# Kernel tuning notes

Measured on AMD Instinct MI355X. Metric: run time of the kernel, lower is better.

## Reference

```python
import jax, jax.numpy as jnp
import numpy as np

C = 256
B = 8
N = 2048
EPS_BN = 1e-5


def _bn(x, g, b):
    # BatchNorm1d in training mode: stats over (batch, length) per channel
    m = x.mean(axis=(0, 2), keepdims=True)
    v = ((x - m) ** 2).mean(axis=(0, 2), keepdims=True)
    return g[None, :, None] * (x - m) / jnp.sqrt(v + EPS_BN) + b[None, :, None]


def _sa_layer(x, wqk, wv, bv, wt, bt, g, b):
    # shared q/k projection (q_conv.weight = k_conv.weight in the original)
    q = jnp.einsum('oc,bcn->bon', wqk, x)          # [B, C//4, N]
    energy = jnp.einsum('bcm,bcn->bmn', q, q)      # x_q^T x_k -> [B, N, N]
    att = jax.nn.softmax(energy, axis=-1)
    att = att / (1e-9 + att.sum(axis=1, keepdims=True))  # L1 renorm over dim=1
    v = jnp.einsum('oc,bcn->bon', wv, x) + bv[None, :, None]
    x_r = jnp.einsum('bcm,bmn->bcn', v, att)       # [B, C, N]
    t = jnp.einsum('oc,bcn->bon', wt, x - x_r) + bt[None, :, None]
    x_r = jax.nn.relu(_bn(t, g, b))
    return x + x_r


def setup_inputs() -> dict:
    key = jax.random.key(0)
    ks = jax.random.split(key, 16)
    s = lambda k, shp, scale: jax.random.normal(k, shp, dtype=jnp.float32) * scale
    inp = {
        'x': s(ks[0], (B, C, N), 1.0),
        'conv1_w': s(ks[1], (C, C), 1.0 / np.sqrt(C)),
        'conv2_w': s(ks[2], (C, C), 1.0 / np.sqrt(C)),
        'bn1_g': jnp.ones((C,), jnp.float32),
        'bn1_b': jnp.zeros((C,), jnp.float32),
        'bn2_g': jnp.ones((C,), jnp.float32),
        'bn2_b': jnp.zeros((C,), jnp.float32),
        'sa_wqk': s(ks[3], (4, C // 4, C), 1.0 / np.sqrt(C)),
        'sa_wv': s(ks[4], (4, C, C), 1.0 / np.sqrt(C)),
        'sa_bv': s(ks[5], (4, C), 0.01),
        'sa_wt': s(ks[6], (4, C, C), 1.0 / np.sqrt(C)),
        'sa_bt': s(ks[7], (4, C), 0.01),
        'sa_g': jnp.ones((4, C), jnp.float32),
        'sa_b': jnp.zeros((4, C), jnp.float32),
    }
    return inp


def reference(x, conv1_w, conv2_w, bn1_g, bn1_b, bn2_g, bn2_b,
              sa_wqk, sa_wv, sa_bv, sa_wt, sa_bt, sa_g, sa_b):
    x = jax.nn.relu(_bn(jnp.einsum('oc,bcn->bon', conv1_w, x), bn1_g, bn1_b))
    x = jax.nn.relu(_bn(jnp.einsum('oc,bcn->bon', conv2_w, x), bn2_g, bn2_b))
    outs = []
    for i in range(4):  # four structurally identical SA layers, small fixed loop
        x = _sa_layer(x, sa_wqk[i], sa_wv[i], sa_bv[i], sa_wt[i], sa_bt[i],
                      sa_g[i], sa_b[i])
        outs.append(x)
    return jnp.concatenate(outs, axis=1)  # [B, 4*C, N]
```

## Files before the change

### kernel.cpp

```cpp
#include <hip/hip_runtime.h>
#include <hip/hip_bf16.h>

typedef __attribute__((ext_vector_type(8))) short short8;
typedef __attribute__((ext_vector_type(4))) float f32x4;
using bf16 = __hip_bfloat16;

constexpr int C  = 256;
constexpr int BB = 8;
constexpr int NN = 2048;

#define DEVI __device__ __forceinline__

DEVI short8 ldg8(const bf16* p) { return *reinterpret_cast<const short8*>(p); }

DEVI f32x4 mfma16(short8 a, short8 b, f32x4 c) {
  return __builtin_amdgcn_mfma_f32_16x16x32_bf16(a, b, c, 0, 0, 0);
}

DEVI void split2(float x, bf16& h, bf16& l) {
  h = __float2bfloat16(x);
  l = __float2bfloat16(x - __bfloat162float(h));
}

DEVI short b2s(bf16 x) { short s; __builtin_memcpy(&s, &x, 2); return s; }


DEVI void store_tile16(const float v[4], bf16* __restrict__ H, bf16* __restrict__ L,
                       size_t tilebase, float* lds, int lane) {
  int l15 = lane & 15, l4 = lane >> 4;
#pragma unroll
  for (int r = 0; r < 4; ++r) lds[(l4 * 4 + r) * 20 + l15] = v[r];
  asm volatile("s_waitcnt lgkmcnt(0)" ::: "memory");
  __builtin_amdgcn_sched_barrier(0);
  int n = lane & 15, cg = (lane >> 4) & 1, pl = lane >> 5;
  short8 o;
#pragma unroll
  for (int j = 0; j < 8; ++j) {
    bf16 h, l;
    split2(lds[n * 20 + cg * 8 + j], h, l);
    o[j] = pl ? b2s(l) : b2s(h);
  }
  bf16* P = pl ? L : H;
  *reinterpret_cast<short8*>(P + tilebase + (size_t)cg * 128 + n * 8) = o;
}

__global__ __launch_bounds__(256) void k_cvtW5(
    const float* __restrict__ s0, const float* __restrict__ s1,
    const float* __restrict__ s2, const float* __restrict__ s3,
    const float* __restrict__ s4, bf16* __restrict__ h0, bf16* __restrict__ l0,
    bf16* __restrict__ h1, bf16* __restrict__ l1, bf16* __restrict__ h2,
    bf16* __restrict__ l2, bf16* __restrict__ h3, bf16* __restrict__ l3,
    bf16* __restrict__ h4, bf16* __restrict__ l4) {
  int idx = blockIdx.x * 256 + threadIdx.x;
  const float* s; bf16 *dh, *dl;
  if (idx < 8192)        { s = s0; dh = h0; dl = l0; }
  else if (idx < 16384)  { s = s1; dh = h1; dl = l1; idx -= 8192; }
  else if (idx < 24576)  { s = s2; dh = h2; dl = l2; idx -= 16384; }
  else if (idx < 57344)  { s = s3; dh = h3; dl = l3; idx -= 24576; }
  else                   { s = s4; dh = h4; dl = l4; idx -= 57344; }
  int row = idx >> 5, kg = idx & 31;
  const float* sp = s + row * 256 + kg * 8;
  short8 oh, ol;
#pragma unroll
  for (int j = 0; j < 8; ++j) {
    bf16 h, l;
    split2(sp[j], h, l);
    oh[j] = b2s(h); ol[j] = b2s(l);
  }
  size_t off = ((size_t)(row >> 4) * 32 + kg) * 128 + (row & 15) * 8;
  *reinterpret_cast<short8*>(dh + off) = oh;
  *reinterpret_cast<short8*>(dl + off) = ol;
}

__global__ __launch_bounds__(256) void k_tin(const float* __restrict__ x,
                                             bf16* __restrict__ Xh,
                                             bf16* __restrict__ Xl) {
  __shared__ float tile[64][65];
  int b = blockIdx.z, n0 = blockIdx.x * 64, c0 = blockIdx.y * 64;
  int t = threadIdx.x;
  int tn = t & 63, tq = t >> 6;
#pragma unroll
  for (int i = 0; i < 16; ++i) {
    int cc = i * 4 + tq;
    tile[cc][tn] = x[((size_t)(b * C + c0 + cc)) * NN + n0 + tn];
  }
  __syncthreads();
  bf16* XHb = Xh + (size_t)b * NN * C;
  bf16* XLb = Xl + (size_t)b * NN * C;
#pragma unroll
  for (int i = 0; i < 4; ++i) {
    int e = i * 256 + t;
    int nl = e & 63;
    int cgp = e >> 6;
    int cg = cgp & 7, pl = cgp >> 3;
    short8 o;
#pragma unroll
    for (int j = 0; j < 8; ++j) {
      bf16 h, l;
      split2(tile[cg * 8 + j][nl], h, l);
      o[j] = pl ? b2s(l) : b2s(h);
    }
    int n = n0 + nl;
    size_t off = ((size_t)(n >> 4) * 32 + ((c0 >> 3) + cg)) * 128 + (n & 15) * 8;
    bf16* P = pl ? XLb : XHb;
    *reinterpret_cast<short8*>(P + off) = o;
  }
}

template <bool BIASJ, bool STATS>
__global__ __launch_bounds__(512, 4) void k_gemm_tr(const bf16* __restrict__ Ah,
                                                    const bf16* __restrict__ Al,
                                                    const bf16* __restrict__ Wh,
                                                    const bf16* __restrict__ Wl,
                                                    const float* __restrict__ bias,
                                                    float* __restrict__ OutF, int OD,
                                                    float* __restrict__ sS,
                                                    float* __restrict__ sS2) {
  __shared__ short8 smW[4096];
  __shared__ float smS[64], smS2[64];
  int b = blockIdx.x, i0 = blockIdx.y * 128, j0 = blockIdx.z * 64;
  int t = threadIdx.x, lane = t & 63, w = t >> 6;
  int l15 = lane & 15, l4 = lane >> 4;
  if (STATS && t < 64) { smS[t] = 0.f; smS2[t] = 0.f; }
  size_t wbase = (size_t)(j0 >> 4) * 4096;
  for (int i = t; i < 2048; i += 512) {
    smW[i]        = ldg8(Wh + wbase + (size_t)i * 8);
    smW[2048 + i] = ldg8(Wl + wbase + (size_t)i * 8);
  }
  __syncthreads();
  const bf16* Abh = Ah + (size_t)b * NN * C;
  const bf16* Abl = Al + (size_t)b * NN * C;
  int ntile = (i0 >> 4) + w;
  f32x4 acc[4];
#pragma unroll
  for (int ct = 0; ct < 4; ++ct) acc[ct] = f32x4{0.f, 0.f, 0.f, 0.f};
#pragma unroll
  for (int ks = 0; ks < 8; ++ks) {
    int ko = ks * 4 + l4;
    short8 a_h = ldg8(Abh + ((size_t)ntile * 32 + ko) * 128 + l15 * 8);
    short8 a_l = ldg8(Abl + ((size_t)ntile * 32 + ko) * 128 + l15 * 8);
#pragma unroll
    for (int ct = 0; ct < 4; ++ct) {
      short8 w_h = smW[ct * 512 + ko * 16 + l15];
      short8 w_l = smW[2048 + ct * 512 + ko * 16 + l15];
      acc[ct] = mfma16(a_h, w_h, acc[ct]);
      acc[ct] = mfma16(a_h, w_l, acc[ct]);
      acc[ct] = mfma16(a_l, w_h, acc[ct]);
    }
  }
#pragma unroll
  for (int ct = 0; ct < 4; ++ct) {
    float bj = 0.f;
    if (BIASJ) bj = bias[j0 + ct * 16 + l15];
    float s = 0.f, s2 = 0.f;
#pragma unroll
    for (int r = 0; r < 4; ++r) {
      float v = acc[ct][r] + bj;
      int row = i0 + w * 16 + l4 * 4 + r;
      OutF[((size_t)(b * NN + row)) * OD + j0 + ct * 16 + l15] = v;
      if (STATS) { s += v; s2 += v * v; }
    }
    if (STATS) {
      s += __shfl_xor(s, 16); s2 += __shfl_xor(s2, 16);
      s += __shfl_xor(s, 32); s2 += __shfl_xor(s2, 32);
      if (l4 == 0) {
        atomicAdd(&smS[ct * 16 + l15], s);
        atomicAdd(&smS2[ct * 16 + l15], s2);
      }
    }
  }
  if (STATS) {
    __syncthreads();
    if (t < 64) {
      atomicAdd(&sS[j0 + t], smS[t]);
      atomicAdd(&sS2[j0 + t], smS2[t]);
    }
  }
}

__global__ __launch_bounds__(256) void k_qproj(const bf16* __restrict__ Xh,
                                               const bf16* __restrict__ Xl,
                                               const bf16* __restrict__ Wh,
                                               const bf16* __restrict__ Wl,
                                               bf16* __restrict__ Qh,
                                               bf16* __restrict__ Ql) {
  __shared__ float scratch[4][320];
  int b = blockIdx.x, ntile = blockIdx.y;
  int t = threadIdx.x, lane = t & 63, w = t >> 6;
  int l15 = lane & 15, l4 = lane >> 4;
  const bf16* Abh = Xh + (size_t)b * NN * C;
  const bf16* Abl = Xl + (size_t)b * NN * C;
  f32x4 acc = {0.f, 0.f, 0.f, 0.f};
#pragma unroll
  for (int ks = 0; ks < 8; ++ks) {
    int ko = ks * 4 + l4;
    short8 a_h = ldg8(Abh + ((size_t)ntile * 32 + ko) * 128 + l15 * 8);
    short8 a_l = ldg8(Abl + ((size_t)ntile * 32 + ko) * 128 + l15 * 8);
    size_t wo = ((size_t)w * 32 + ko) * 128 + l15 * 8;
    short8 w_h = ldg8(Wh + wo);
    short8 w_l = ldg8(Wl + wo);
    acc = mfma16(a_h, w_h, acc);
    acc = mfma16(a_h, w_l, acc);
    acc = mfma16(a_l, w_h, acc);
  }
  float v[4] = {acc[0], acc[1], acc[2], acc[3]};
  size_t tb = ((size_t)ntile * 8 + w * 2) * 128;
  store_tile16(v, Qh + (size_t)b * NN * 64, Ql + (size_t)b * NN * 64, tb,
               scratch[w], lane);
}

__global__ __launch_bounds__(512, 4) void k_gemm_nm(const bf16* __restrict__ Wh,
                                                    const bf16* __restrict__ Wl,
                                                    const bf16* __restrict__ Xh,
                                                    const bf16* __restrict__ Xl,
                                                    const float* __restrict__ bias,
                                                    bf16* __restrict__ Vh,
                                                    bf16* __restrict__ Vl) {
  __shared__ short8 smX[4096];
  __shared__ float scratch[8][320];
  int b = blockIdx.x, i0 = blockIdx.y * 128, j0 = blockIdx.z * 64;
  int t = threadIdx.x, lane = t & 63, w = t >> 6;
  int l15 = lane & 15, l4 = lane >> 4;
  const bf16* Xbh = Xh + (size_t)b * NN * C;
  const bf16* Xbl = Xl + (size_t)b * NN * C;
  size_t xbase = (size_t)(j0 >> 4) * 4096;
  for (int i = t; i < 2048; i += 512) {
    smX[i]        = ldg8(Xbh + xbase + (size_t)i * 8);
    smX[2048 + i] = ldg8(Xbl + xbase + (size_t)i * 8);
  }
  __syncthreads();
  int ntile = (i0 >> 4) + w;
  f32x4 acc[4];
#pragma unroll
  for (int ct = 0; ct < 4; ++ct) acc[ct] = f32x4{0.f, 0.f, 0.f, 0.f};
#pragma unroll
  for (int ks = 0; ks < 8; ++ks) {
    int ko = ks * 4 + l4;
    short8 a_h = ldg8(Wh + ((size_t)ntile * 32 + ko) * 128 + l15 * 8);
    short8 a_l = ldg8(Wl + ((size_t)ntile * 32 + ko) * 128 + l15 * 8);
#pragma unroll
    for (int ct = 0; ct < 4; ++ct) {
      short8 x_h = smX[ct * 512 + ko * 16 + l15];
      short8 x_l = smX[2048 + ct * 512 + ko * 16 + l15];
      acc[ct] = mfma16(a_h, x_h, acc[ct]);
      acc[ct] = mfma16(a_h, x_l, acc[ct]);
      acc[ct] = mfma16(a_l, x_h, acc[ct]);
    }
  }
  float br[4];
#pragma unroll
  for (int r = 0; r < 4; ++r) br[r] = bias[i0 + w * 16 + l4 * 4 + r];
  bf16* Vbh = Vh + (size_t)b * C * NN;
  bf16* Vbl = Vl + (size_t)b * C * NN;
#pragma unroll
  for (int ct = 0; ct < 4; ++ct) {
    float v[4];
#pragma unroll
    for (int r = 0; r < 4; ++r) v[r] = acc[ct][r] + br[r];
    size_t tb = ((size_t)ntile * (NN >> 3) + ((j0 + ct * 16) >> 3)) * 128;
    store_tile16(v, Vbh, Vbl, tb, scratch[w], lane);
  }
}

__global__ __launch_bounds__(256) void k_rowstats(const bf16* __restrict__ Qh,
                                                  const bf16* __restrict__ Ql,
                                                  float* __restrict__ rm,
                                                  float* __restrict__ irs) {
  __shared__ float redM[4][16], redS[4][16];
  int b = blockIdx.x;
  int t = threadIdx.x, lane = t & 63, w = t >> 6;
  int l15 = lane & 15, l4 = lane >> 4;
  int mt = blockIdx.y;
  const bf16* QHb = Qh + (size_t)b * NN * 64;
  const bf16* QLb = Ql + (size_t)b * NN * 64;
  short8 ah0 = ldg8(QHb + ((size_t)mt * 8 + l4) * 128 + l15 * 8);
  short8 ah1 = ldg8(QHb + ((size_t)mt * 8 + 4 + l4) * 128 + l15 * 8);
  short8 al0 = ldg8(QLb + ((size_t)mt * 8 + l4) * 128 + l15 * 8);
  short8 al1 = ldg8(QLb + ((size_t)mt * 8 + 4 + l4) * 128 + l15 * 8);
  float lmax[4], lsum[4];
#pragma unroll
  for (int r = 0; r < 4; ++r) { lmax[r] = -3.4e38f; lsum[r] = 0.f; }
  for (int nb = w * 32; nb < w * 32 + 32; ++nb) {
    short8 bh0 = ldg8(QHb + ((size_t)nb * 8 + l4) * 128 + l15 * 8);
    short8 bh1 = ldg8(QHb + ((size_t)nb * 8 + 4 + l4) * 128 + l15 * 8);
    short8 bl0 = ldg8(QLb + ((size_t)nb * 8 + l4) * 128 + l15 * 8);
    short8 bl1 = ldg8(QLb + ((size_t)nb * 8 + 4 + l4) * 128 + l15 * 8);
    f32x4 e = {0.f, 0.f, 0.f, 0.f};
    e = mfma16(ah0, bh0, e); e = mfma16(ah1, bh1, e);
    e = mfma16(ah0, bl0, e); e = mfma16(ah1, bl1, e);
    e = mfma16(al0, bh0, e); e = mfma16(al1, bh1, e);
#pragma unroll
    for (int r = 0; r < 4; ++r) {
      float v = e[r];
      float nm = fmaxf(lmax[r], v);
      lsum[r] = lsum[r] * __expf(lmax[r] - nm) + __expf(v - nm);
      lmax[r] = nm;
    }
  }
#pragma unroll
  for (int r = 0; r < 4; ++r) {
    for (int mk = 1; mk < 16; mk <<= 1) {
      float om = __shfl_xor(lmax[r], mk, 16);
      float os = __shfl_xor(lsum[r], mk, 16);
      float nm = fmaxf(lmax[r], om);
      lsum[r] = lsum[r] * __expf(lmax[r] - nm) + os * __expf(om - nm);
      lmax[r] = nm;
    }
  }
  if (l15 == 0) {
#pragma unroll
    for (int r = 0; r < 4; ++r) {
      redM[w][l4 * 4 + r] = lmax[r];
      redS[w][l4 * 4 + r] = lsum[r];
    }
  }
  __syncthreads();
  if (t < 16) {
    float m = redM[0][t];
    m = fmaxf(m, redM[1][t]); m = fmaxf(m, redM[2][t]); m = fmaxf(m, redM[3][t]);
    float s = 0.f;
#pragma unroll
    for (int w2 = 0; w2 < 4; ++w2) s += redS[w2][t] * __expf(redM[w2][t] - m);
    rm[b * NN + mt * 16 + t] = m;
    irs[b * NN + mt * 16 + t] = 1.0f / s;
  }
}

__global__ __launch_bounds__(512, 4) void k_attnY(const bf16* __restrict__ QH,
                                                  const bf16* __restrict__ QL,
                                                  const bf16* __restrict__ VH,
                                                  const bf16* __restrict__ VL,
                                                  const float* __restrict__ rm,
                                                  const float* __restrict__ irs,
                                                  const bf16* __restrict__ XH,
                                                  const bf16* __restrict__ XL,
                                                  bf16* __restrict__ DH,
                                                  bf16* __restrict__ DL) {
  __shared__ bf16 Pb[2][32 * 136];
  __shared__ float rmL[2048], irL[2048];
  __shared__ float colLds[32];
  __shared__ float scratch[8][320];
  int bid = blockIdx.x;
  int b = bid & 7, n0 = (bid >> 3) * 32;
  int t = threadIdx.x, lane = t & 63, w = t >> 6;
  int l15 = lane & 15, l4 = lane >> 4;
  int nt = w >> 2, pp = w & 3;
  const bf16* QHb = QH + (size_t)b * NN * 64;
  const bf16* QLb = QL + (size_t)b * NN * 64;
  const bf16* VHb = VH + (size_t)b * C * NN;
  const bf16* VLb = VL + (size_t)b * C * NN;
  for (int i = t; i < NN; i += 512) {
    rmL[i] = rm[b * NN + i];
    irL[i] = irs[b * NN + i];
  }
  if (t < 32) colLds[t] = 0.f;
  int ntq = (n0 >> 4) + nt;
  short8 qh0 = ldg8(QHb + ((size_t)ntq * 8 + l4) * 128 + l15 * 8);
  short8 qh1 = ldg8(QHb + ((size_t)ntq * 8 + 4 + l4) * 128 + l15 * 8);
  short8 ql0 = ldg8(QLb + ((size_t)ntq * 8 + l4) * 128 + l15 * 8);
  short8 ql1 = ldg8(QLb + ((size_t)ntq * 8 + 4 + l4) * 128 + l15 * 8);
  f32x4 zero = {0.f, 0.f, 0.f, 0.f};
  f32x4 acc[2][2];
#pragma unroll
  for (int a = 0; a < 2; ++a)
#pragma unroll
    for (int ct = 0; ct < 2; ++ct) acc[a][ct] = zero;
  float cac[4] = {0.f, 0.f, 0.f, 0.f};
  __syncthreads();
  for (int s = 0; s < 16; ++s) {
    bf16* pbw = Pb[s & 1];
#pragma unroll
    for (int sub = 0; sub < 2; ++sub) {
      int mt8 = pp * 2 + sub;
      int gmt = s * 8 + mt8;
      short8 bh0 = ldg8(QHb + ((size_t)gmt * 8 + l4) * 128 + l15 * 8);
      short8 bh1 = ldg8(QHb + ((size_t)gmt * 8 + 4 + l4) * 128 + l15 * 8);
      short8 bl0 = ldg8(QLb + ((size_t)gmt * 8 + l4) * 128 + l15 * 8);
      short8 bl1 = ldg8(QLb + ((size_t)gmt * 8 + 4 + l4) * 128 + l15 * 8);
      f32x4 eA = zero, eB = zero;
      eA = mfma16(qh0, bh0, eA); eB = mfma16(qh1, bh1, eB);
      eA = mfma16(qh0, bl0, eA); eB = mfma16(qh1, bl1, eB);
      eA = mfma16(ql0, bh0, eA); eB = mfma16(ql1, bh1, eB);
      float rmv = rmL[gmt * 16 + l15], iv = irL[gmt * 16 + l15];
      int blk = nt * 16 + mt8 * 2 + (l15 >> 3);
#pragma unroll
      for (int r = 0; r < 4; ++r) {
        float p = __expf(eA[r] + eB[r] - rmv) * iv;
        bf16 ph = __float2bfloat16(p);
        cac[r] += __bfloat162float(ph);
        pbw[blk * 136 + (l4 * 4 + r) * 8 + (l15 & 7)] = ph;
      }
    }
    short8 vhA[2][2], vlA[2][2];
#pragma unroll
    for (int kc = 0; kc < 2; ++kc)
#pragma unroll
      for (int ct = 0; ct < 2; ++ct) {
        size_t vo = ((size_t)(w * 2 + ct) * 256 + s * 16 + kc * 4 + l4) * 128 + l15 * 8;
        vhA[kc][ct] = ldg8(VHb + vo);
        vlA[kc][ct] = ldg8(VLb + vo);
      }
    asm volatile("s_waitcnt lgkmcnt(0)" ::: "memory");
    __builtin_amdgcn_sched_barrier(0);
    __builtin_amdgcn_s_barrier();
    short8 vhB[2][2], vlB[2][2];
#pragma unroll
    for (int kc = 0; kc < 2; ++kc)
#pragma unroll
      for (int ct = 0; ct < 2; ++ct) {
        size_t vo = ((size_t)(w * 2 + ct) * 256 + s * 16 + (kc + 2) * 4 + l4) * 128 + l15 * 8;
        vhB[kc][ct] = ldg8(VHb + vo);
        vlB[kc][ct] = ldg8(VLb + vo);
      }
#pragma unroll
    for (int kc = 0; kc < 2; ++kc) {
      short8 pa0 = *reinterpret_cast<const short8*>(&pbw[(kc * 4 + l4) * 136 + l15 * 8]);
      short8 pa1 = *reinterpret_cast<const short8*>(&pbw[(16 + kc * 4 + l4) * 136 + l15 * 8]);
#pragma unroll
      for (int ct = 0; ct < 2; ++ct) {
        acc[0][ct] = mfma16(pa0, vhA[kc][ct], acc[0][ct]);
        acc[0][ct] = mfma16(pa0, vlA[kc][ct], acc[0][ct]);
        acc[1][ct] = mfma16(pa1, vhA[kc][ct], acc[1][ct]);
        acc[1][ct] = mfma16(pa1, vlA[kc][ct], acc[1][ct]);
      }
    }
#pragma unroll
    for (int kc = 0; kc < 2; ++kc) {
      short8 pa0 = *reinterpret_cast<const short8*>(&pbw[((kc + 2) * 4 + l4) * 136 + l15 * 8]);
      short8 pa1 = *reinterpret_cast<const short8*>(&pbw[(16 + (kc + 2) * 4 + l4) * 136 + l15 * 8]);
#pragma unroll
      for (int ct = 0; ct < 2; ++ct) {
        acc[0][ct] = mfma16(pa0, vhB[kc][ct], acc[0][ct]);
        acc[0][ct] = mfma16(pa0, vlB[kc][ct], acc[0][ct]);
        acc[1][ct] = mfma16(pa1, vhB[kc][ct], acc[1][ct]);
        acc[1][ct] = mfma16(pa1, vlB[kc][ct], acc[1][ct]);
      }
    }
  }
#pragma unroll
  for (int r = 0; r < 4; ++r) {
    float v2 = cac[r];
    v2 += __shfl_xor(v2, 1, 16); v2 += __shfl_xor(v2, 2, 16);
    v2 += __shfl_xor(v2, 4, 16); v2 += __shfl_xor(v2, 8, 16);
    if (l15 == 0) atomicAdd(&colLds[nt * 16 + l4 * 4 + r], v2);
  }
  __syncthreads();
  if (t < 32) colLds[t] = 1.0f / (1e-9f + colLds[t]);
  __syncthreads();
  const bf16* XHb = XH + (size_t)b * NN * C;
  const bf16* XLb = XL + (size_t)b * NN * C;
  bf16* DHb = DH + (size_t)b * NN * C;
  bf16* DLb = DL + (size_t)b * NN * C;
#pragma unroll
  for (int a = 0; a < 2; ++a) {
#pragma unroll
    for (int ct = 0; ct < 2; ++ct) {
      float d[4];
      int cidx = w * 32 + ct * 16 + l15;
#pragma unroll
      for (int r = 0; r < 4; ++r) {
        int n = n0 + a * 16 + l4 * 4 + r;
        size_t off = ((size_t)(n >> 4) * 32 + (cidx >> 3)) * 128 + (n & 15) * 8 + (cidx & 7);
        float xv = __bfloat162float(XHb[off]) + __bfloat162float(XLb[off]);
        d[r] = xv - acc[a][ct][r] * colLds[a * 16 + l4 * 4 + r];
      }
      size_t tb = ((size_t)((n0 >> 4) + a) * 32 + ((w * 32 + ct * 16) >> 3)) * 128;
      store_tile16(d, DHb, DLb, tb, scratch[w], lane);
    }
  }
}

template <bool RES>
__global__ __launch_bounds__(256) void k_bnrelu(const float* __restrict__ Tt,
                                                const float* __restrict__ sS,
                                                const float* __restrict__ sS2,
                                                const float* __restrict__ g,
                                                const float* __restrict__ bb,
                                                bf16* __restrict__ Xh,
                                                bf16* __restrict__ Xl,
                                                float* __restrict__ outp, int Loff) {
  __shared__ float vb[16][257];
  int b = blockIdx.x, n0 = blockIdx.y * 16;
  int c = threadIdx.x;
  float cnt = (float)(BB * NN);
  float mean = sS[c] / cnt;
  float var = fmaxf(sS2[c] / cnt - mean * mean, 0.f);
  float sc = g[c] * rsqrtf(var + 1e-5f);
  float sh = bb[c] - mean * sc;
#pragma unroll
  for (int i = 0; i < 16; ++i) {
    int n = n0 + i;
    size_t idx = ((size_t)(b * NN + n)) * C + c;
    float v = Tt[idx] * sc + sh;
    v = fmaxf(v, 0.f);
    size_t off = (size_t)b * NN * C +
                 ((size_t)(n >> 4) * 32 + (c >> 3)) * 128 + (n & 15) * 8 + (c & 7);
    if (RES) v += __bfloat162float(Xh[off]) + __bfloat162float(Xl[off]);
    bf16 h, l;
    split2(v, h, l);
    Xh[off] = h;
    Xl[off] = l;
    if (RES) vb[i][c] = v;
  }
  if (RES) {
    __syncthreads();
    int nl = threadIdx.x & 15, cb = threadIdx.x >> 4;
#pragma unroll
    for (int j = 0; j < 16; ++j) {
      int cc = cb + j * 16;
      outp[((size_t)(b * 1024 + Loff + cc)) * NN + n0 + nl] = vb[nl][cc];
    }
  }
}

extern "C" void kernel_launch(void* const* d_in, const int* in_sizes, int n_in,
                              void* d_out, int out_size, void* d_ws, size_t ws_size,
                              hipStream_t stream) {
  const float* x       = (const float*)d_in[0];
  const float* conv1_w = (const float*)d_in[1];
  const float* conv2_w = (const float*)d_in[2];
  const float* bn1_g   = (const float*)d_in[3];
  const float* bn1_b   = (const float*)d_in[4];
  const float* bn2_g   = (const float*)d_in[5];
  const float* bn2_b   = (const float*)d_in[6];
  const float* wqk     = (const float*)d_in[7];
  const float* wv      = (const float*)d_in[8];
  const float* bv      = (const float*)d_in[9];
  const float* wt      = (const float*)d_in[10];
  const float* bt      = (const float*)d_in[11];
  const float* sg      = (const float*)d_in[12];
  const float* sb      = (const float*)d_in[13];
  float* out = (float*)d_out;

  char* p = (char*)d_ws;
  auto take = [&](size_t n) { char* r = p; p += n; return r; };
  bf16* WB1h = (bf16*)take(131072);
  bf16* WB1l = (bf16*)take(131072);
  bf16* WB2h = (bf16*)take(131072);
  bf16* WB2l = (bf16*)take(131072);
  bf16* WBQh = (bf16*)take(131072);
  bf16* WBQl = (bf16*)take(131072);
  bf16* WBVh = (bf16*)take(524288);
  bf16* WBVl = (bf16*)take(524288);
  bf16* WBTh = (bf16*)take(524288);
  bf16* WBTl = (bf16*)take(524288);
  bf16* XTh  = (bf16*)take(8388608);
  bf16* XTl  = (bf16*)take(8388608);
  bf16* QTh  = (bf16*)take(2097152);
  bf16* QTl  = (bf16*)take(2097152);
  bf16* VBh  = (bf16*)take(8388608);
  bf16* VBl  = (bf16*)take(8388608);
  float* TT  = (float*)VBh;
  bf16* DTh  = (bf16*)take(8388608);
  bf16* DTl  = (bf16*)take(8388608);
  float* RM   = (float*)take(65536);
  float* IRS  = (float*)take(65536);
  float* STAT = (float*)take(12288);

  hipMemsetAsync(STAT, 0, 6 * 512 * sizeof(float), stream);
  k_cvtW5<<<352, 256, 0, stream>>>(conv1_w, conv2_w, wqk, wv, wt,
                                   WB1h, WB1l, WB2h, WB2l, WBQh, WBQl,
                                   WBVh, WBVl, WBTh, WBTl);
  k_tin<<<dim3(32, 4, 8), 256, 0, stream>>>(x, XTh, XTl);

  k_gemm_tr<false, true><<<dim3(8, 16, 4), 512, 0, stream>>>(
      XTh, XTl, WB1h, WB1l, nullptr, TT, 256, STAT + 0, STAT + 256);
  k_bnrelu<false><<<dim3(8, 128), 256, 0, stream>>>(TT, STAT + 0, STAT + 256, bn1_g, bn1_b,
                                                    XTh, XTl, nullptr, 0);

  k_gemm_tr<false, true><<<dim3(8, 16, 4), 512, 0, stream>>>(
      XTh, XTl, WB2h, WB2l, nullptr, TT, 256, STAT + 512, STAT + 768);
  k_bnrelu<false><<<dim3(8, 128), 256, 0, stream>>>(TT, STAT + 512, STAT + 768, bn2_g, bn2_b,
                                                    XTh, XTl, nullptr, 0);

  for (int L = 0; L < 4; ++L) {
    float* ST = STAT + (2 + L) * 512;
    k_qproj<<<dim3(8, 128), 256, 0, stream>>>(XTh, XTl, WBQh + L * 16384,
                                              WBQl + L * 16384, QTh, QTl);
    k_gemm_nm<<<dim3(8, 2, 32), 512, 0, stream>>>(WBVh + L * 65536, WBVl + L * 65536,
                                                  XTh, XTl, bv + L * 256, VBh, VBl);
    k_rowstats<<<dim3(8, 128), 256, 0, stream>>>(QTh, QTl, RM, IRS);
    k_attnY<<<512, 512, 0, stream>>>(QTh, QTl, VBh, VBl, RM, IRS, XTh, XTl, DTh, DTl);
    k_gemm_tr<true, true><<<dim3(8, 16, 4), 512, 0, stream>>>(
        DTh, DTl, WBTh + L * 65536, WBTl + L * 65536, bt + L * 256, TT, 256, ST, ST + 256);
    k_bnrelu<true><<<dim3(8, 128), 256, 0, stream>>>(TT, ST, ST + 256, sg + L * 256,
                                                     sb + L * 256, XTh, XTl, out,
                                                     L * 256);
  }
}
```

Measured before the change: 628.2 us.

## Double attention key-tile per step, software-pipeline V loads, unroll rowstats loop by two

In k_attnY each outer step now covers 256 keys instead of 128, halving the number of block barriers, and the P staging buffer grows to hold 64 rows. V fragments are loaded one k-chunk ahead in a rolling register pipeline instead of being batched into two half-step groups. Occupancy hint drops from 4 to 2 blocks per CU, accepting more LDS and register use. k_rowstats processes two key tiles per iteration to raise MFMA and load ILP and to cut online-softmax rescale work.

```diff
diff --git a/kernel.cpp b/kernel.cpp
--- a/kernel.cpp
+++ b/kernel.cpp
@@ -280,20 +280,26 @@
   float lmax[4], lsum[4];
 #pragma unroll
   for (int r = 0; r < 4; ++r) { lmax[r] = -3.4e38f; lsum[r] = 0.f; }
-  for (int nb = w * 32; nb < w * 32 + 32; ++nb) {
+  for (int nb = w * 32; nb < w * 32 + 32; nb += 2) {
     short8 bh0 = ldg8(QHb + ((size_t)nb * 8 + l4) * 128 + l15 * 8);
     short8 bh1 = ldg8(QHb + ((size_t)nb * 8 + 4 + l4) * 128 + l15 * 8);
     short8 bl0 = ldg8(QLb + ((size_t)nb * 8 + l4) * 128 + l15 * 8);
     short8 bl1 = ldg8(QLb + ((size_t)nb * 8 + 4 + l4) * 128 + l15 * 8);
-    f32x4 e = {0.f, 0.f, 0.f, 0.f};
-    e = mfma16(ah0, bh0, e); e = mfma16(ah1, bh1, e);
-    e = mfma16(ah0, bl0, e); e = mfma16(ah1, bl1, e);
-    e = mfma16(al0, bh0, e); e = mfma16(al1, bh1, e);
+    short8 ch0 = ldg8(QHb + ((size_t)(nb + 1) * 8 + l4) * 128 + l15 * 8);
+    short8 ch1 = ldg8(QHb + ((size_t)(nb + 1) * 8 + 4 + l4) * 128 + l15 * 8);
+    short8 cl0 = ldg8(QLb + ((size_t)(nb + 1) * 8 + l4) * 128 + l15 * 8);
+    short8 cl1 = ldg8(QLb + ((size_t)(nb + 1) * 8 + 4 + l4) * 128 + l15 * 8);
+    f32x4 e1 = {0.f, 0.f, 0.f, 0.f}, e2 = {0.f, 0.f, 0.f, 0.f};
+    e1 = mfma16(ah0, bh0, e1); e1 = mfma16(ah1, bh1, e1);
+    e1 = mfma16(ah0, bl0, e1); e1 = mfma16(ah1, bl1, e1);
+    e1 = mfma16(al0, bh0, e1); e1 = mfma16(al1, bh1, e1);
+    e2 = mfma16(ah0, ch0, e2); e2 = mfma16(ah1, ch1, e2);
+    e2 = mfma16(ah0, cl0, e2); e2 = mfma16(ah1, cl1, e2);
+    e2 = mfma16(al0, ch0, e2); e2 = mfma16(al1, ch1, e2);
 #pragma unroll
     for (int r = 0; r < 4; ++r) {
-      float v = e[r];
-      float nm = fmaxf(lmax[r], v);
-      lsum[r] = lsum[r] * __expf(lmax[r] - nm) + __expf(v - nm);
+      float nm = fmaxf(lmax[r], fmaxf(e1[r], e2[r]));
+      lsum[r] = lsum[r] * __expf(lmax[r] - nm) + __expf(e1[r] - nm) + __expf(e2[r] - nm);
       lmax[r] = nm;
     }
   }
@@ -326,7 +332,7 @@
   }
 }
 
-__global__ __launch_bounds__(512, 4) void k_attnY(const bf16* __restrict__ QH,
+__global__ __launch_bounds__(512, 2) void k_attnY(const bf16* __restrict__ QH,
                                                   const bf16* __restrict__ QL,
                                                   const bf16* __restrict__ VH,
                                                   const bf16* __restrict__ VL,
@@ -336,7 +342,7 @@
                                                   const bf16* __restrict__ XL,
                                                   bf16* __restrict__ DH,
                                                   bf16* __restrict__ DL) {
-  __shared__ bf16 Pb[2][32 * 136];
+  __shared__ bf16 Pb[2][64 * 136];
   __shared__ float rmL[2048], irL[2048];
   __shared__ float colLds[32];
   __shared__ float scratch[8][320];
@@ -367,12 +373,12 @@
     for (int ct = 0; ct < 2; ++ct) acc[a][ct] = zero;
   float cac[4] = {0.f, 0.f, 0.f, 0.f};
   __syncthreads();
-  for (int s = 0; s < 16; ++s) {
+  for (int s = 0; s < 8; ++s) {
     bf16* pbw = Pb[s & 1];
 #pragma unroll
-    for (int sub = 0; sub < 2; ++sub) {
-      int mt8 = pp * 2 + sub;
-      int gmt = s * 8 + mt8;
+    for (int sub = 0; sub < 4; ++sub) {
+      int mt16 = pp * 4 + sub;
+      int gmt = s * 16 + mt16;
       short8 bh0 = ldg8(QHb + ((size_t)gmt * 8 + l4) * 128 + l15 * 8);
       short8 bh1 = ldg8(QHb + ((size_t)gmt * 8 + 4 + l4) * 128 + l15 * 8);
       short8 bl0 = ldg8(QLb + ((size_t)gmt * 8 + l4) * 128 + l15 * 8);
@@ -382,7 +388,7 @@
       eA = mfma16(qh0, bl0, eA); eB = mfma16(qh1, bl1, eB);
       eA = mfma16(ql0, bh0, eA); eB = mfma16(ql1, bh1, eB);
       float rmv = rmL[gmt * 16 + l15], iv = irL[gmt * 16 + l15];
-      int blk = nt * 16 + mt8 * 2 + (l15 >> 3);
+      int blk = nt * 32 + mt16 * 2 + (l15 >> 3);
 #pragma unroll
       for (int r = 0; r < 4; ++r) {
         float p = __expf(eA[r] + eB[r] - rmv) * iv;
@@ -391,50 +397,37 @@
         pbw[blk * 136 + (l4 * 4 + r) * 8 + (l15 & 7)] = ph;
       }
     }
-    short8 vhA[2][2], vlA[2][2];
-#pragma unroll
-    for (int kc = 0; kc < 2; ++kc)
-#pragma unroll
-      for (int ct = 0; ct < 2; ++ct) {
-        size_t vo = ((size_t)(w * 2 + ct) * 256 + s * 16 + kc * 4 + l4) * 128 + l15 * 8;
-        vhA[kc][ct] = ldg8(VHb + vo);
-        vlA[kc][ct] = ldg8(VLb + vo);
-      }
+    short8 vch[2], vcl[2], vnh[2], vnl[2];
+#pragma unroll
+    for (int ct = 0; ct < 2; ++ct) {
+      size_t vo = ((size_t)(w * 2 + ct) * 256 + s * 32 + l4) * 128 + l15 * 8;
+      vch[ct] = ldg8(VHb + vo);
+      vcl[ct] = ldg8(VLb + vo);
+    }
     asm volatile("s_waitcnt lgkmcnt(0)" ::: "memory");
     __builtin_amdgcn_sched_barrier(0);
     __builtin_amdgcn_s_barrier();
-    short8 vhB[2][2], vlB[2][2];
-#pragma unroll
-    for (int kc = 0; kc < 2; ++kc)
+#pragma unroll
+    for (int kc = 0; kc < 8; ++kc) {
+      if (kc < 7) {
+#pragma unroll
+        for (int ct = 0; ct < 2; ++ct) {
+          size_t vo = ((size_t)(w * 2 + ct) * 256 + s * 32 + (kc + 1) * 4 + l4) * 128 + l15 * 8;
+          vnh[ct] = ldg8(VHb + vo);
+          vnl[ct] = ldg8(VLb + vo);
+        }
+      }
+      short8 pa0 = *reinterpret_cast<const short8*>(&pbw[(kc * 4 + l4) * 136 + l15 * 8]);
+      short8 pa1 = *reinterpret_cast<const short8*>(&pbw[((32 + kc * 4 + l4)) * 136 + l15 * 8]);
 #pragma unroll
       for (int ct = 0; ct < 2; ++ct) {
-        size_t vo = ((size_t)(w * 2 + ct) * 256 + s * 16 + (kc + 2) * 4 + l4) * 128 + l15 * 8;
-        vhB[kc][ct] = ldg8(VHb + vo);
-        vlB[kc][ct] = ldg8(VLb + vo);
+        acc[0][ct] = mfma16(pa0, vch[ct], acc[0][ct]);
+        acc[0][ct] = mfma16(pa0, vcl[ct], acc[0][ct]);
+        acc[1][ct] = mfma16(pa1, vch[ct], acc[1][ct]);
+        acc[1][ct] = mfma16(pa1, vcl[ct], acc[1][ct]);
       }
 #pragma unroll
-    for (int kc = 0; kc < 2; ++kc) {
-      short8 pa0 = *reinterpret_cast<const short8*>(&pbw[(kc * 4 + l4) * 136 + l15 * 8]);
-      short8 pa1 = *reinterpret_cast<const short8*>(&pbw[(16 + kc * 4 + l4) * 136 + l15 * 8]);
-#pragma unroll
-      for (int ct = 0; ct < 2; ++ct) {
-        acc[0][ct] = mfma16(pa0, vhA[kc][ct], acc[0][ct]);
-        acc[0][ct] = mfma16(pa0, vlA[kc][ct], acc[0][ct]);
-        acc[1][ct] = mfma16(pa1, vhA[kc][ct], acc[1][ct]);
-        acc[1][ct] = mfma16(pa1, vlA[kc][ct], acc[1][ct]);
-      }
-    }
-#pragma unroll
-    for (int kc = 0; kc < 2; ++kc) {
-      short8 pa0 = *reinterpret_cast<const short8*>(&pbw[((kc + 2) * 4 + l4) * 136 + l15 * 8]);
-      short8 pa1 = *reinterpret_cast<const short8*>(&pbw[(16 + (kc + 2) * 4 + l4) * 136 + l15 * 8]);
-#pragma unroll
-      for (int ct = 0; ct < 2; ++ct) {
-        acc[0][ct] = mfma16(pa0, vhB[kc][ct], acc[0][ct]);
-        acc[0][ct] = mfma16(pa0, vlB[kc][ct], acc[0][ct]);
-        acc[1][ct] = mfma16(pa1, vhB[kc][ct], acc[1][ct]);
-        acc[1][ct] = mfma16(pa1, vlB[kc][ct], acc[1][ct]);
-      }
+      for (int ct = 0; ct < 2; ++ct) { vch[ct] = vnh[ct]; vcl[ct] = vnl[ct]; }
     }
   }
 #pragma unroll
```

New measurement: 801.6 us. 1.28x slower.
